# Kernel tuning notes

Measured on AMD Instinct MI355X. Metric: run time of the kernel, lower is better.

Reference implementation:

```python
import jax, jax.numpy as jnp
import numpy as np
from jax import lax

B, N, T, D_IN, D_OUT, LINK_LEN, EMBED = 32, 500, 12, 1, 64, 3, 10
C_WIN = 1            # x_window feature dim ((dim_in-1)%16==0 branch)
CNN_CH = D_OUT // 16  # 4 channels per topology CNN


def setup_inputs() -> dict:
    key = jax.random.key(0)
    ks = jax.random.split(key, 16)
    s = 0.1
    inp = {}
    inp["x"] = jax.random.normal(ks[0], (B, N, D_IN), jnp.float32)
    inp["x_window"] = jax.random.normal(ks[1], (B, T, N, C_WIN), jnp.float32)
    inp["node_embeddings"] = jax.random.normal(ks[2], (N, EMBED), jnp.float32)
    inp["adj"] = jax.random.uniform(ks[3], (N, N), jnp.float32)
    inp["MPG"] = jax.random.normal(ks[4], (B, T, N, N), jnp.float32)
    inp["bootstrap_idx"] = jnp.sort(jax.random.randint(ks[5], (3,), 0, T))
    inp["fixed_adj"] = 0
    inp["stay_cost"] = 1
    inp["jump_cost"] = 2
    inp["weights_pool"] = jax.random.normal(ks[6], (EMBED, LINK_LEN, D_IN, 3 * D_OUT // 4), jnp.float32) * s
    inp["window_weights_supra"] = jax.random.normal(ks[7], (EMBED, C_WIN, D_OUT // 8), jnp.float32) * s
    inp["window_weights_temporal"] = jax.random.normal(ks[8], (EMBED, C_WIN, D_OUT // 8), jnp.float32) * s
    inp["bias_pool"] = jax.random.normal(ks[9], (EMBED, D_OUT), jnp.float32) * s
    inp["T_param"] = jax.random.normal(ks[10], (T,), jnp.float32) * s
    inp["conv_mean_w"] = jax.random.normal(ks[11], (CNN_CH, T, 3, 3), jnp.float32) * s
    inp["conv_mean_b"] = jnp.zeros((CNN_CH,), jnp.float32)
    inp["conv_max_w"] = jax.random.normal(ks[12], (CNN_CH, T, 3, 3), jnp.float32) * s
    inp["conv_max_b"] = jnp.zeros((CNN_CH,), jnp.float32)
    return inp


def _conv2d(x, w, b):
    y = lax.conv_general_dilated(x, w, (1, 1), 'SAME',
                                 dimension_numbers=('NCHW', 'OIHW', 'NCHW'))
    return y + b[None, :, None, None]


def reference(x, x_window, node_embeddings, adj, MPG, bootstrap_idx, fixed_adj,
              stay_cost, jump_cost, weights_pool, window_weights_supra,
              window_weights_temporal, bias_pool, T_param,
              conv_mean_w, conv_mean_b, conv_max_w, conv_max_b):
    n = node_embeddings.shape[0]
    eye = jnp.eye(n, dtype=x.dtype)
    # adaptive adjacency from node embeddings, diagonal set to stay_cost
    s0 = jax.nn.relu(node_embeddings @ node_embeddings.T)
    s0 = jnp.where(eye > 0, jnp.asarray(stay_cost, x.dtype), s0)
    if fixed_adj == 1:
        S = adj * jnp.exp(s0)
    else:
        S = jax.nn.softmax(s0, axis=1)
    # faithful to torch broadcast: S[i,j] / sum_k S[j,k]
    S = S / jnp.sum(S, axis=1)
    # multi-hop supports: I, S, S@S, ...
    supports = [eye, S]
    for k in range(2, LINK_LEN):
        supports.append(S @ supports[-1])
    supports = jnp.stack(supports, axis=0)  # [K, N, N]
    # supra-laplacian: diagonal blocks S, strictly-upper blocks jump_cost*I
    F_b = bootstrap_idx.shape[0]  # 3 bootstrap layers
    supra = (jnp.kron(jnp.eye(F_b, dtype=x.dtype), S)
             + jnp.kron(jnp.triu(jnp.ones((F_b, F_b), x.dtype), 1),
                        jnp.asarray(jump_cost, x.dtype) * eye))
    # node-adaptive weights/bias
    weights = jnp.einsum('nd,dkio->nkio', node_embeddings, weights_pool)
    bias = node_embeddings @ bias_pool  # [N, D_OUT]
    # spatial graph conv
    x_s = jnp.einsum('knm,bmc->bnkc', supports, x)
    x_sconv = jnp.einsum('bnki,nkio->bno', x_s, weights)  # [B,N,48]
    # supra-laplacian window conv over bootstrap slices
    ww_s = jnp.einsum('nd,dio->nio', node_embeddings, window_weights_supra)
    xw = x_window[:, bootstrap_idx]            # [B, 3, N, c]
    b_sz = xw.shape[0]
    xw_flat = xw.reshape(b_sz, F_b * n, -1)    # [B, 3N, c]
    xws = jnp.einsum('bmi,mn->bni', xw_flat, supra).reshape(b_sz, F_b, n, -1)
    x_wconv_s = jnp.einsum('bfni,nio->bfno', xws, ww_s).mean(axis=1)  # [B,N,8]
    # temporal window conv
    ww_t = jnp.einsum('nd,dio->nio', node_embeddings, window_weights_temporal)
    x_wconv_t = jnp.einsum('btni,nio,t->bno', x_window, ww_t, T_param)  # [B,N,8]
    # topology CNNs (conv + relu + global mean / max pool)
    topo_mean = jax.nn.relu(_conv2d(MPG, conv_mean_w, conv_mean_b)).mean(axis=(2, 3))
    topo_max = jax.nn.relu(_conv2d(MPG, conv_max_w, conv_max_b)).max(axis=(2, 3))
    topo = jnp.concatenate([topo_mean, topo_max], axis=1)  # [B, 8]
    x_twconv_s = x_wconv_s * topo[:, None, :]
    return jnp.concatenate([x_sconv, x_twconv_s, x_wconv_t], axis=-1) + bias[None]
```

## Files before the change

### kernel.cpp

```cpp
#include <hip/hip_runtime.h>

#define NN 500
#define BB 32
#define TT 12
#define EMB 10

typedef short bf16x8 __attribute__((ext_vector_type(8)));
typedef float f32x16 __attribute__((ext_vector_type(16)));

__device__ __forceinline__ unsigned short f2bf(float x) {
    unsigned int u = __float_as_uint(x);
    u = (u + 0x7fffu + ((u >> 16) & 1u)) >> 16;
    return (unsigned short)u;
}

__global__ __launch_bounds__(256) void k_softmaxS(const float* __restrict__ E,
                                                  const int* __restrict__ stay,
                                                  float* __restrict__ S) {
    const int i = blockIdx.x;
    const int tid = threadIdx.x;
    __shared__ float row[NN];
    __shared__ float red[256];
    float ei[EMB];
#pragma unroll
    for (int d = 0; d < EMB; ++d) ei[d] = E[i * EMB + d];
    const float stayf = (float)stay[0];

    float lmax = -1e30f;
    for (int j = tid; j < NN; j += 256) {
        float acc = 0.f;
#pragma unroll
        for (int d = 0; d < EMB; ++d) acc += ei[d] * E[j * EMB + d];
        float v = acc > 0.f ? acc : 0.f;
        if (j == i) v = stayf;
        row[j] = v;
        lmax = fmaxf(lmax, v);
    }
    red[tid] = lmax;
    __syncthreads();
    for (int s = 128; s > 0; s >>= 1) {
        if (tid < s) red[tid] = fmaxf(red[tid], red[tid + s]);
        __syncthreads();
    }
    const float rmax = red[0];
    __syncthreads();

    float lsum = 0.f;
    for (int j = tid; j < NN; j += 256) {
        float e = __expf(row[j] - rmax);
        row[j] = e;
        lsum += e;
    }
    red[tid] = lsum;
    __syncthreads();
    for (int s = 128; s > 0; s >>= 1) {
        if (tid < s) red[tid] += red[tid + s];
        __syncthreads();
    }
    const float inv = 1.0f / red[0];
    for (int j = tid; j < NN; j += 256) S[i * NN + j] = row[j] * inv;
}

__global__ __launch_bounds__(256) void k_matvecS(const float* __restrict__ S,
                                                 const float* __restrict__ xin,
                                                 float* __restrict__ yout) {
    const int b = blockIdx.y;
    const int w = threadIdx.x >> 6;
    const int lane = threadIdx.x & 63;
    const int n = blockIdx.x * 4 + w;
    const float* xb = xin + b * NN;
    const float* Sr = S + n * NN;
    float acc = 0.f;
    for (int m = lane; m < NN; m += 64) acc += Sr[m] * xb[m];
#pragma unroll
    for (int off = 32; off > 0; off >>= 1) acc += __shfl_down(acc, off, 64);
    if (lane == 0) yout[b * NN + n] = acc;
}

__global__ __launch_bounds__(256) void k_smallpre(const float* __restrict__ E,
                                                  const float* __restrict__ wp,
                                                  const float* __restrict__ bp,
                                                  const float* __restrict__ wwsp,
                                                  const float* __restrict__ wwtp,
                                                  float* __restrict__ W,
                                                  float* __restrict__ biasN,
                                                  float* __restrict__ wws,
                                                  float* __restrict__ wwt) {
    const int n = blockIdx.x;
    const int tid = threadIdx.x;
    __shared__ float e[EMB];
    if (tid < EMB) e[tid] = E[n * EMB + tid];
    __syncthreads();
    if (tid < 144) {
        float acc = 0.f;
#pragma unroll
        for (int d = 0; d < EMB; ++d) acc += e[d] * wp[d * 144 + tid];
        W[n * 144 + tid] = acc;
    } else if (tid < 208) {
        const int o = tid - 144;
        float acc = 0.f;
#pragma unroll
        for (int d = 0; d < EMB; ++d) acc += e[d] * bp[d * 64 + o];
        biasN[n * 64 + o] = acc;
    } else if (tid < 216) {
        const int o = tid - 208;
        float acc = 0.f;
#pragma unroll
        for (int d = 0; d < EMB; ++d) acc += e[d] * wwsp[d * 8 + o];
        wws[n * 8 + o] = acc;
    } else if (tid < 224) {
        const int o = tid - 216;
        float acc = 0.f;
#pragma unroll
        for (int d = 0; d < EMB; ++d) acc += e[d] * wwtp[d * 8 + o];
        wwt[n * 8 + o] = acc;
    }
}

__global__ __launch_bounds__(128) void k_Mwsum(const float* __restrict__ xwin,
                                               const float* __restrict__ S,
                                               const int* __restrict__ bidx,
                                               const int* __restrict__ jumpc,
                                               const float* __restrict__ Tp,
                                               float* __restrict__ M,
                                               float* __restrict__ wsum) {
    const int b = blockIdx.y;
    const int n0 = blockIdx.x * 125;
    const int tid = threadIdx.x;
    __shared__ float xsf[NN];
    __shared__ float Tl[TT];
    const int t0 = bidx[0], t1 = bidx[1], t2 = bidx[2];
    if (tid < TT) Tl[tid] = Tp[tid];
    const float* xb = xwin + (size_t)b * TT * NN;
    for (int m = tid; m < NN; m += 128)
        xsf[m] = xb[t0 * NN + m] + xb[t1 * NN + m] + xb[t2 * NN + m];
    __syncthreads();
    if (tid < 125) {
        const int n = n0 + tid;
        float ws_ = 0.f;
#pragma unroll
        for (int t = 0; t < TT; ++t) ws_ += xb[t * NN + n] * Tl[t];
        const float jc = (float)jumpc[0];
        const float jterm = jc * (2.f * xb[t0 * NN + n] + xb[t1 * NN + n]);
        float acc = 0.f;
        for (int m = 0; m < NN; ++m) acc += xsf[m] * S[m * NN + n];
        M[b * NN + n] = (acc + jterm) * (1.f / 3.f);
        wsum[b * NN + n] = ws_;
    }
}

__global__ __launch_bounds__(256) void k_wpackB(const float* __restrict__ wm,
                                                const float* __restrict__ wx,
                                                unsigned short* __restrict__ wq) {
    const int i = blockIdx.x * 256 + threadIdx.x;
    if (i >= 9 * 64 * 8) return;
    const int j = i & 7;
    const int rest = i >> 3;
    const int lane = rest & 63;
    const int s = rest >> 6;
    const int kh = s / 3, kw = s - kh * 3;
    const int n = lane & 31;
    const int t = (lane >> 5) * 8 + j;
    float v = 0.f;
    if (t < TT) {
        if (n < 4) v = wm[((n * TT + t) * 3 + kh) * 3 + kw];
        else if (n < 8) v = wx[(((n - 4) * TT + t) * 3 + kh) * 3 + kw];
    }
    wq[i] = f2bf(v);
}

#define SLOTW 132
#define SLOTS (SLOTW * 24)
#define SLOTW32 (SLOTW * 12)

__global__ __launch_bounds__(256, 2) void k_conv(const float* __restrict__ MPG,
                                                 const unsigned short* __restrict__ wq,
                                                 const float* __restrict__ bmv,
                                                 const float* __restrict__ bxv,
                                                 float* __restrict__ partials) {
    const int b = blockIdx.y;
    const int cb = blockIdx.x >> 3;
    const int rb = blockIdx.x & 7;
    const int C0 = cb * 128;
    const int R0 = rb * 63;
    const int R1 = (R0 + 62 < NN - 1) ? R0 + 62 : NN - 1;
    const int tid = threadIdx.x;
    const int w = __builtin_amdgcn_readfirstlane(tid >> 6);
    const int lane = tid & 63;
    const int hi = lane >> 5;

    __shared__ unsigned short lsd[4 * SLOTS];
    __shared__ float wred[4][8][2];

    const float* basef = MPG + (size_t)b * TT * NN * NN;
    unsigned int* L32 = reinterpret_cast<unsigned int*>(lsd);

    bf16x8 bfq[9];
#pragma unroll
    for (int s = 0; s < 9; ++s)
        bfq[s] = *reinterpret_cast<const bf16x8*>(wq + (s * 64 + lane) * 8);

    bool uval[4], uco[4];
    size_t g0[4];
    int ud[4];
#pragma unroll
    for (int k = 0; k < 4; ++k) {
        const int f = tid + k * 256;
        uval[k] = (f < 6 * SLOTW);
        const int tp = uval[k] ? (f / SLOTW) : 0;
        const int sc = uval[k] ? (f - tp * SLOTW) : 0;
        const int gcol = C0 - 1 + sc;
        uco[k] = uval[k] && (gcol >= 0) && (gcol < NN);
        g0[k] = (size_t)(2 * tp) * (NN * NN) + (uco[k] ? gcol : 0);
        ud[k] = sc * 12 + tp;
    }

    for (int z = tid; z < 4 * SLOTW; z += 256) {
        const int s = z / SLOTW;
        const int sc = z - s * SLOTW;
        L32[s * SLOTW32 + sc * 12 + 6] = 0u;
        L32[s * SLOTW32 + sc * 12 + 7] = 0u;
    }

    const int ch = lane & 31;
    const float biasv = (ch < 4) ? bmv[ch] : ((ch < 8) ? bxv[ch - 4] : 0.f);
    const bool interior = (C0 + w * 32 + 31) < NN;
    float mkv[16];
#pragma unroll
    for (int i = 0; i < 16; ++i) {
        const int p = C0 + w * 32 + (i & 3) + 8 * (i >> 2) + 4 * hi;
        mkv[i] = (p < NN) ? 1.f : 0.f;
    }
    const int aoff = (w * 32 + ch) * 48 + hi * 16;

    auto STAGE_LOAD = [&](int rr, float (&v0)[4], float (&v1)[4]) {
        const bool rowok = (rr >= 0) && (rr < NN);
#pragma unroll
        for (int k = 0; k < 4; ++k) {
            v0[k] = 0.f; v1[k] = 0.f;
            if (uco[k] && rowok) {
                const size_t o = g0[k] + (size_t)rr * NN;
                v0[k] = basef[o];
                v1[k] = basef[o + (size_t)NN * NN];
            }
        }
    };
    auto STAGE_WRITE = [&](int rr, const float (&v0)[4], const float (&v1)[4]) {
        unsigned int* dst = L32 + ((rr + 1) & 3) * SLOTW32;
#pragma unroll
        for (int k = 0; k < 4; ++k) {
            if (uval[k]) {
                unsigned int r;
                asm("v_cvt_pk_bf16_f32 %0, %1, %2" : "=v"(r) : "v"(v0[k]), "v"(v1[k]));
                dst[ud[k]] = r;
            }
        }
    };

#pragma unroll
    for (int q = 0; q < 3; ++q) {
        float v0[4], v1[4];
        STAGE_LOAD(R0 - 1 + q, v0, v1);
        STAGE_WRITE(R0 - 1 + q, v0, v1);
    }
    __syncthreads();

    float sumv = 0.f, maxv = 0.f;

#pragma unroll 1
    for (int r = R0; r <= R1; ++r) {
        const int rr = r + 2;
        const bool do_stage = (rr <= R1 + 1);
        float v0[4], v1[4];
        if (do_stage) STAGE_LOAD(rr, v0, v1);

        f32x16 acc;
#pragma unroll
        for (int i = 0; i < 16; ++i) acc[i] = biasv;
#pragma unroll
        for (int kh = 0; kh < 3; ++kh) {
            const char* sb = reinterpret_cast<const char*>(lsd) + ((r + kh) & 3) * (SLOTS * 2);
#pragma unroll
            for (int kw = 0; kw < 3; ++kw) {
                const bf16x8 a = *reinterpret_cast<const bf16x8*>(sb + aoff + kw * 48);
                acc = __builtin_amdgcn_mfma_f32_32x32x16_bf16(a, bfq[kh * 3 + kw], acc, 0, 0, 0);
            }
        }

        if (interior) {
            float rs = 0.f;
#pragma unroll
            for (int i = 0; i < 16; ++i) rs += fmaxf(acc[i], 0.f);
            sumv += rs;
            float mm = acc[0];
#pragma unroll
            for (int i = 1; i < 16; ++i) mm = fmaxf(mm, acc[i]);
            maxv = fmaxf(maxv, mm);
        } else {
#pragma unroll
            for (int i = 0; i < 16; ++i) {
                const float v = fmaxf(acc[i], 0.f) * mkv[i];
                sumv += v;
                maxv = fmaxf(maxv, v);
            }
        }

        if (do_stage) STAGE_WRITE(rr, v0, v1);
        __syncthreads();
    }

    sumv += __shfl_xor(sumv, 32, 64);
    maxv = fmaxf(maxv, __shfl_xor(maxv, 32, 64));
    if (lane < 8) {
        wred[w][lane][0] = sumv;
        wred[w][lane][1] = maxv;
    }
    __syncthreads();
    if (tid < 8) {
        const float s = wred[0][tid][0] + wred[1][tid][0] + wred[2][tid][0] + wred[3][tid][0];
        const float mx = fmaxf(fmaxf(wred[0][tid][1], wred[1][tid][1]),
                               fmaxf(wred[2][tid][1], wred[3][tid][1]));
        partials[((size_t)b * 32 + blockIdx.x) * 8 + tid] = (tid < 4) ? s : mx;
    }
}

__global__ __launch_bounds__(256) void k_topo(const float* __restrict__ partials,
                                              float* __restrict__ topo) {
    const int b = blockIdx.x;
    const int tid = threadIdx.x;
    const int c = tid & 7;
    const int g = tid >> 3;
    float vs = 0.f, vm = 0.f;
    if (g < 32) {
        const float v = partials[((size_t)b * 32 + g) * 8 + c];
        vs = v;
        vm = v;
    }
    __shared__ float red[256];
    red[tid] = (c < 4) ? vs : vm;
    __syncthreads();
    for (int s = 16; s > 0; s >>= 1) {
        if (g < s) {
            const float a = red[tid];
            const float bv = red[tid + s * 8];
            red[tid] = (c < 4) ? (a + bv) : fmaxf(a, bv);
        }
        __syncthreads();
    }
    if (tid < 8) topo[b * 8 + tid] = (tid < 4) ? red[tid] * (1.f / (NN * (float)NN)) : red[tid];
}

__global__ __launch_bounds__(64) void k_out(const float* __restrict__ x,
                                            const float* __restrict__ y1,
                                            const float* __restrict__ y2,
                                            const float* __restrict__ W,
                                            const float* __restrict__ biasN,
                                            const float* __restrict__ wws,
                                            const float* __restrict__ wwt,
                                            const float* __restrict__ M,
                                            const float* __restrict__ wsum,
                                            const float* __restrict__ topo,
                                            float* __restrict__ out) {
    const int bn = blockIdx.x;
    const int b = bn / NN;
    const int n = bn - b * NN;
    const int o = threadIdx.x;
    float val;
    if (o < 48) {
        val = x[bn] * W[n * 144 + o] + y1[bn] * W[n * 144 + 48 + o] + y2[bn] * W[n * 144 + 96 + o];
    } else if (o < 56) {
        const int oo = o - 48;
        val = M[bn] * wws[n * 8 + oo] * topo[b * 8 + oo];
    } else {
        const int oo = o - 56;
        val = wsum[bn] * wwt[n * 8 + oo];
    }
    out[(size_t)bn * 64 + o] = val + biasN[n * 64 + o];
}

extern "C" void kernel_launch(void* const* d_in, const int* in_sizes, int n_in,
                              void* d_out, int out_size, void* d_ws, size_t ws_size,
                              hipStream_t stream) {
    const float* x    = (const float*)d_in[0];
    const float* xw   = (const float*)d_in[1];
    const float* E    = (const float*)d_in[2];
    const float* MPG  = (const float*)d_in[4];
    const int*   bidx = (const int*)d_in[5];
    const int*   stay = (const int*)d_in[7];
    const int*   jump = (const int*)d_in[8];
    const float* wp   = (const float*)d_in[9];
    const float* wwsp = (const float*)d_in[10];
    const float* wwtp = (const float*)d_in[11];
    const float* bp   = (const float*)d_in[12];
    const float* Tp   = (const float*)d_in[13];
    const float* cmw  = (const float*)d_in[14];
    const float* cmb  = (const float*)d_in[15];
    const float* cxw  = (const float*)d_in[16];
    const float* cxb  = (const float*)d_in[17];
    float* out = (float*)d_out;

    float* w = (float*)d_ws;
    float* S     = w;
    float* y1    = S + 250000;
    float* y2    = y1 + 16000;
    float* W     = y2 + 16000;
    float* biasN = W + 72000;
    float* wws   = biasN + 32000;
    float* wwt   = wws + 4000;
    float* M     = wwt + 4000;
    float* wsum  = M + 16000;
    float* parts = wsum + 16000;
    float* topo  = parts + 8192;
    float* wpckf = topo + 256;
    unsigned short* wq = (unsigned short*)wpckf;

    k_wpackB<<<18, 256, 0, stream>>>(cmw, cxw, wq);
    k_softmaxS<<<NN, 256, 0, stream>>>(E, stay, S);
    k_matvecS<<<dim3(125, BB), 256, 0, stream>>>(S, x, y1);
    k_matvecS<<<dim3(125, BB), 256, 0, stream>>>(S, y1, y2);
    k_smallpre<<<NN, 256, 0, stream>>>(E, wp, bp, wwsp, wwtp, W, biasN, wws, wwt);
    k_Mwsum<<<dim3(4, BB), 128, 0, stream>>>(xw, S, bidx, jump, Tp, M, wsum);
    k_conv<<<dim3(32, BB), 256, 0, stream>>>(MPG, wq, cmb, cxb, parts);
    k_topo<<<BB, 256, 0, stream>>>(parts, topo);
    k_out<<<BB * NN, 64, 0, stream>>>(x, y1, y2, W, biasN, wws, wwt, M, wsum, topo, out);
}
```

Baseline: 140.4 us.

## Process three output rows per iteration with an 8-slot LDS ring

The conv loop now computes three output rows per iteration. It loads five input rows of LDS fragments once and reuses them across the three rows' 27 MFMAs, and it stages three new rows per iteration. This cuts LDS reads and per-row barriers by about a factor of three. The last row block is shifted to start at NN-63 so every block runs exactly 21 iterations, and rows already covered by the previous block are masked out. In exchange, LDS use doubles to 8 slots, register pressure rises from holding 15 fragments plus 12 staged loads, and occupancy at two blocks per CU may be affected.

```diff
diff --git a/kernel.cpp b/kernel.cpp
--- a/kernel.cpp
+++ b/kernel.cpp
@@ -171,6 +171,7 @@
 
 #define SLOTW 132
 #define SLOTS (SLOTW * 24)
+#define SLOTB (SLOTS * 2)
 #define SLOTW32 (SLOTW * 12)
 
 __global__ __launch_bounds__(256, 2) void k_conv(const float* __restrict__ MPG,
@@ -182,14 +183,14 @@
     const int cb = blockIdx.x >> 3;
     const int rb = blockIdx.x & 7;
     const int C0 = cb * 128;
-    const int R0 = rb * 63;
-    const int R1 = (R0 + 62 < NN - 1) ? R0 + 62 : NN - 1;
+    const int rmin = rb * 63;
+    const int R0 = (rb < 7) ? rb * 63 : (NN - 63);
     const int tid = threadIdx.x;
     const int w = __builtin_amdgcn_readfirstlane(tid >> 6);
     const int lane = tid & 63;
     const int hi = lane >> 5;
 
-    __shared__ unsigned short lsd[4 * SLOTS];
+    __shared__ unsigned short lsd[8 * SLOTS];
     __shared__ float wred[4][8][2];
 
     const float* basef = MPG + (size_t)b * TT * NN * NN;
@@ -215,7 +216,7 @@
         ud[k] = sc * 12 + tp;
     }
 
-    for (int z = tid; z < 4 * SLOTW; z += 256) {
+    for (int z = tid; z < 8 * SLOTW; z += 256) {
         const int s = z / SLOTW;
         const int sc = z - s * SLOTW;
         L32[s * SLOTW32 + sc * 12 + 6] = 0u;
@@ -246,7 +247,7 @@
         }
     };
     auto STAGE_WRITE = [&](int rr, const float (&v0)[4], const float (&v1)[4]) {
-        unsigned int* dst = L32 + ((rr + 1) & 3) * SLOTW32;
+        unsigned int* dst = L32 + ((rr + 1) & 7) * SLOTW32;
 #pragma unroll
         for (int k = 0; k < 4; ++k) {
             if (uval[k]) {
@@ -258,7 +259,7 @@
     };
 
 #pragma unroll
-    for (int q = 0; q < 3; ++q) {
+    for (int q = 0; q < 5; ++q) {
         float v0[4], v1[4];
         STAGE_LOAD(R0 - 1 + q, v0, v1);
         STAGE_WRITE(R0 - 1 + q, v0, v1);
@@ -268,44 +269,64 @@
     float sumv = 0.f, maxv = 0.f;
 
 #pragma unroll 1
-    for (int r = R0; r <= R1; ++r) {
-        const int rr = r + 2;
-        const bool do_stage = (rr <= R1 + 1);
-        float v0[4], v1[4];
-        if (do_stage) STAGE_LOAD(rr, v0, v1);
-
-        f32x16 acc;
-#pragma unroll
-        for (int i = 0; i < 16; ++i) acc[i] = biasv;
-#pragma unroll
-        for (int kh = 0; kh < 3; ++kh) {
-            const char* sb = reinterpret_cast<const char*>(lsd) + ((r + kh) & 3) * (SLOTS * 2);
-#pragma unroll
-            for (int kw = 0; kw < 3; ++kw) {
-                const bf16x8 a = *reinterpret_cast<const bf16x8*>(sb + aoff + kw * 48);
-                acc = __builtin_amdgcn_mfma_f32_32x32x16_bf16(a, bfq[kh * 3 + kw], acc, 0, 0, 0);
+    for (int k21 = 0; k21 < 21; ++k21) {
+        const int r = R0 + 3 * k21;
+        const bool do_stage = (k21 < 20);
+
+        float v0[3][4], v1[3][4];
+        if (do_stage) {
+#pragma unroll
+            for (int q = 0; q < 3; ++q) STAGE_LOAD(r + 4 + q, v0[q], v1[q]);
+        }
+
+        bf16x8 F[5][3];
+#pragma unroll
+        for (int j = 0; j < 5; ++j) {
+            const char* sb = reinterpret_cast<const char*>(lsd) + ((r + j) & 7) * SLOTB;
+#pragma unroll
+            for (int kw = 0; kw < 3; ++kw)
+                F[j][kw] = *reinterpret_cast<const bf16x8*>(sb + aoff + kw * 48);
+        }
+
+#pragma unroll
+        for (int o = 0; o < 3; ++o) {
+            f32x16 acc;
+#pragma unroll
+            for (int i = 0; i < 16; ++i) acc[i] = biasv;
+#pragma unroll
+            for (int kh = 0; kh < 3; ++kh) {
+#pragma unroll
+                for (int kw = 0; kw < 3; ++kw)
+                    acc = __builtin_amdgcn_mfma_f32_32x32x16_bf16(F[o + kh][kw], bfq[kh * 3 + kw], acc, 0, 0, 0);
             }
-        }
-
-        if (interior) {
-            float rs = 0.f;
-#pragma unroll
-            for (int i = 0; i < 16; ++i) rs += fmaxf(acc[i], 0.f);
-            sumv += rs;
-            float mm = acc[0];
-#pragma unroll
-            for (int i = 1; i < 16; ++i) mm = fmaxf(mm, acc[i]);
-            maxv = fmaxf(maxv, mm);
-        } else {
-#pragma unroll
-            for (int i = 0; i < 16; ++i) {
-                const float v = fmaxf(acc[i], 0.f) * mkv[i];
-                sumv += v;
-                maxv = fmaxf(maxv, v);
+            const int ro = r + o;
+            if (interior && (ro >= rmin)) {
+                float rs = 0.f;
+#pragma unroll
+                for (int i = 0; i < 16; ++i) rs += fmaxf(acc[i], 0.f);
+                sumv += rs;
+                float mm = acc[0];
+#pragma unroll
+                for (int i = 1; i < 16; ++i) mm = fmaxf(mm, acc[i]);
+                maxv = fmaxf(maxv, mm);
+            } else {
+                const float rm = (ro >= rmin) ? 1.f : 0.f;
+                float rs = 0.f, rx = 0.f;
+#pragma unroll
+                for (int i = 0; i < 16; ++i) {
+                    const float v = fmaxf(acc[i], 0.f) * mkv[i];
+                    rs += v;
+                    rx = fmaxf(rx, v);
+                }
+                sumv += rm * rs;
+                maxv = fmaxf(maxv, rm * rx);
             }
         }
 
-        if (do_stage) STAGE_WRITE(rr, v0, v1);
+        if (do_stage) {
+#pragma unroll
+            for (int q = 0; q < 3; ++q) STAGE_WRITE(r + 4 + q, v0[q], v1[q]);
+        }
         __syncthreads();
     }
 
```

Result: slower. 153.7 us (+9.4%).

## Merge small preprocessing kernels into combined launches and split conv reduction accumulators

Applied to the files above, without the earlier changes.

Combines softmax adjacency, per-node weight generation and conv weight packing into one kernel selected by block index. It also folds the first matvec and the M/wsum computation into a single launch, cutting the launch count from nine to six. Separately, the conv epilogue now keeps 16 independent sum and max accumulators per lane instead of serial chains, shortening dependency chains at the cost of extra registers. The extra registers may reduce occupancy in k_conv, which is declared with launch bounds of 2 blocks.

```diff
diff --git a/kernel.cpp b/kernel.cpp
--- a/kernel.cpp
+++ b/kernel.cpp
@@ -14,51 +14,158 @@
     return (unsigned short)u;
 }
 
-__global__ __launch_bounds__(256) void k_softmaxS(const float* __restrict__ E,
-                                                  const int* __restrict__ stay,
-                                                  float* __restrict__ S) {
-    const int i = blockIdx.x;
+__global__ __launch_bounds__(256) void k_pre(const float* __restrict__ E,
+                                             const int* __restrict__ stay,
+                                             const float* __restrict__ wp,
+                                             const float* __restrict__ bp,
+                                             const float* __restrict__ wwsp,
+                                             const float* __restrict__ wwtp,
+                                             const float* __restrict__ wm,
+                                             const float* __restrict__ wx,
+                                             float* __restrict__ S,
+                                             float* __restrict__ W,
+                                             float* __restrict__ biasN,
+                                             float* __restrict__ wws,
+                                             float* __restrict__ wwt,
+                                             unsigned short* __restrict__ wq) {
+    const int bid = blockIdx.x;
     const int tid = threadIdx.x;
-    __shared__ float row[NN];
-    __shared__ float red[256];
-    float ei[EMB];
-#pragma unroll
-    for (int d = 0; d < EMB; ++d) ei[d] = E[i * EMB + d];
-    const float stayf = (float)stay[0];
-
-    float lmax = -1e30f;
-    for (int j = tid; j < NN; j += 256) {
+    if (bid < NN) {
+        __shared__ float row[NN];
+        __shared__ float red[256];
+        const int i = bid;
+        float ei[EMB];
+#pragma unroll
+        for (int d = 0; d < EMB; ++d) ei[d] = E[i * EMB + d];
+        const float stayf = (float)stay[0];
+
+        float lmax = -1e30f;
+        for (int j = tid; j < NN; j += 256) {
+            float acc = 0.f;
+#pragma unroll
+            for (int d = 0; d < EMB; ++d) acc += ei[d] * E[j * EMB + d];
+            float v = acc > 0.f ? acc : 0.f;
+            if (j == i) v = stayf;
+            row[j] = v;
+            lmax = fmaxf(lmax, v);
+        }
+        red[tid] = lmax;
+        __syncthreads();
+        for (int s = 128; s > 0; s >>= 1) {
+            if (tid < s) red[tid] = fmaxf(red[tid], red[tid + s]);
+            __syncthreads();
+        }
+        const float rmax = red[0];
+        __syncthreads();
+
+        float lsum = 0.f;
+        for (int j = tid; j < NN; j += 256) {
+            float e = __expf(row[j] - rmax);
+            row[j] = e;
+            lsum += e;
+        }
+        red[tid] = lsum;
+        __syncthreads();
+        for (int s = 128; s > 0; s >>= 1) {
+            if (tid < s) red[tid] += red[tid + s];
+            __syncthreads();
+        }
+        const float inv = 1.0f / red[0];
+        for (int j = tid; j < NN; j += 256) S[i * NN + j] = row[j] * inv;
+    } else if (bid < 2 * NN) {
+        const int n = bid - NN;
+        __shared__ float e[EMB];
+        if (tid < EMB) e[tid] = E[n * EMB + tid];
+        __syncthreads();
+        if (tid < 144) {
+            float acc = 0.f;
+#pragma unroll
+            for (int d = 0; d < EMB; ++d) acc += e[d] * wp[d * 144 + tid];
+            W[n * 144 + tid] = acc;
+        } else if (tid < 208) {
+            const int o = tid - 144;
+            float acc = 0.f;
+#pragma unroll
+            for (int d = 0; d < EMB; ++d) acc += e[d] * bp[d * 64 + o];
+            biasN[n * 64 + o] = acc;
+        } else if (tid < 216) {
+            const int o = tid - 208;
+            float acc = 0.f;
+#pragma unroll
+            for (int d = 0; d < EMB; ++d) acc += e[d] * wwsp[d * 8 + o];
+            wws[n * 8 + o] = acc;
+        } else if (tid < 224) {
+            const int o = tid - 216;
+            float acc = 0.f;
+#pragma unroll
+            for (int d = 0; d < EMB; ++d) acc += e[d] * wwtp[d * 8 + o];
+            wwt[n * 8 + o] = acc;
+        }
+    } else {
+        const int i = (bid - 2 * NN) * 256 + tid;
+        if (i < 9 * 64 * 8) {
+            const int j = i & 7;
+            const int rest = i >> 3;
+            const int lane = rest & 63;
+            const int s = rest >> 6;
+            const int kh = s / 3, kw = s - kh * 3;
+            const int n = lane & 31;
+            const int t = (lane >> 5) * 8 + j;
+            float v = 0.f;
+            if (t < TT) {
+                if (n < 4) v = wm[((n * TT + t) * 3 + kh) * 3 + kw];
+                else if (n < 8) v = wx[(((n - 4) * TT + t) * 3 + kh) * 3 + kw];
+            }
+            wq[i] = f2bf(v);
+        }
+    }
+}
+
+__global__ __launch_bounds__(256) void k_mv1(const float* __restrict__ S,
+                                             const float* __restrict__ x,
+                                             const float* __restrict__ xwin,
+                                             const int* __restrict__ bidx,
+                                             const int* __restrict__ jumpc,
+                                             const float* __restrict__ Tp,
+                                             float* __restrict__ y1,
+                                             float* __restrict__ M,
+                                             float* __restrict__ wsum) {
+    const int b = blockIdx.y;
+    const int tid = threadIdx.x;
+    if (blockIdx.x < 125) {
+        const int w = tid >> 6;
+        const int lane = tid & 63;
+        const int n = blockIdx.x * 4 + w;
+        const float* xb = x + b * NN;
+        const float* Sr = S + n * NN;
         float acc = 0.f;
-#pragma unroll
-        for (int d = 0; d < EMB; ++d) acc += ei[d] * E[j * EMB + d];
-        float v = acc > 0.f ? acc : 0.f;
-        if (j == i) v = stayf;
-        row[j] = v;
-        lmax = fmaxf(lmax, v);
-    }
-    red[tid] = lmax;
-    __syncthreads();
-    for (int s = 128; s > 0; s >>= 1) {
-        if (tid < s) red[tid] = fmaxf(red[tid], red[tid + s]);
-        __syncthreads();
-    }
-    const float rmax = red[0];
-    __syncthreads();
-
-    float lsum = 0.f;
-    for (int j = tid; j < NN; j += 256) {
-        float e = __expf(row[j] - rmax);
-        row[j] = e;
-        lsum += e;
-    }
-    red[tid] = lsum;
-    __syncthreads();
-    for (int s = 128; s > 0; s >>= 1) {
-        if (tid < s) red[tid] += red[tid + s];
-        __syncthreads();
-    }
-    const float inv = 1.0f / red[0];
-    for (int j = tid; j < NN; j += 256) S[i * NN + j] = row[j] * inv;
+        for (int m = lane; m < NN; m += 64) acc += Sr[m] * xb[m];
+#pragma unroll
+        for (int off = 32; off > 0; off >>= 1) acc += __shfl_down(acc, off, 64);
+        if (lane == 0) y1[b * NN + n] = acc;
+    } else {
+        const int n0 = (blockIdx.x - 125) * 125;
+        __shared__ float xsf[NN];
+        __shared__ float Tl[TT];
+        const int t0 = bidx[0], t1 = bidx[1], t2 = bidx[2];
+        if (tid < TT) Tl[tid] = Tp[tid];
+        const float* xb = xwin + (size_t)b * TT * NN;
+        for (int m = tid; m < NN; m += 256)
+            xsf[m] = xb[t0 * NN + m] + xb[t1 * NN + m] + xb[t2 * NN + m];
+        __syncthreads();
+        if (tid < 125) {
+            const int n = n0 + tid;
+            float ws_ = 0.f;
+#pragma unroll
+            for (int t = 0; t < TT; ++t) ws_ += xb[t * NN + n] * Tl[t];
+            const float jc = (float)jumpc[0];
+            const float jterm = jc * (2.f * xb[t0 * NN + n] + xb[t1 * NN + n]);
+            float acc = 0.f;
+            for (int m = 0; m < NN; ++m) acc += xsf[m] * S[m * NN + n];
+            M[b * NN + n] = (acc + jterm) * (1.f / 3.f);
+            wsum[b * NN + n] = ws_;
+        }
+    }
 }
 
 __global__ __launch_bounds__(256) void k_matvecS(const float* __restrict__ S,
@@ -75,98 +182,6 @@
 #pragma unroll
     for (int off = 32; off > 0; off >>= 1) acc += __shfl_down(acc, off, 64);
     if (lane == 0) yout[b * NN + n] = acc;
-}
-
-__global__ __launch_bounds__(256) void k_smallpre(const float* __restrict__ E,
-                                                  const float* __restrict__ wp,
-                                                  const float* __restrict__ bp,
-                                                  const float* __restrict__ wwsp,
-                                                  const float* __restrict__ wwtp,
-                                                  float* __restrict__ W,
-                                                  float* __restrict__ biasN,
-                                                  float* __restrict__ wws,
-                                                  float* __restrict__ wwt) {
-    const int n = blockIdx.x;
-    const int tid = threadIdx.x;
-    __shared__ float e[EMB];
-    if (tid < EMB) e[tid] = E[n * EMB + tid];
-    __syncthreads();
-    if (tid < 144) {
-        float acc = 0.f;
-#pragma unroll
-        for (int d = 0; d < EMB; ++d) acc += e[d] * wp[d * 144 + tid];
-        W[n * 144 + tid] = acc;
-    } else if (tid < 208) {
-        const int o = tid - 144;
-        float acc = 0.f;
-#pragma unroll
-        for (int d = 0; d < EMB; ++d) acc += e[d] * bp[d * 64 + o];
-        biasN[n * 64 + o] = acc;
-    } else if (tid < 216) {
-        const int o = tid - 208;
-        float acc = 0.f;
-#pragma unroll
-        for (int d = 0; d < EMB; ++d) acc += e[d] * wwsp[d * 8 + o];
-        wws[n * 8 + o] = acc;
-    } else if (tid < 224) {
-        const int o = tid - 216;
-        float acc = 0.f;
-#pragma unroll
-        for (int d = 0; d < EMB; ++d) acc += e[d] * wwtp[d * 8 + o];
-        wwt[n * 8 + o] = acc;
-    }
-}
-
-__global__ __launch_bounds__(128) void k_Mwsum(const float* __restrict__ xwin,
-                                               const float* __restrict__ S,
-                                               const int* __restrict__ bidx,
-                                               const int* __restrict__ jumpc,
-                                               const float* __restrict__ Tp,
-                                               float* __restrict__ M,
-                                               float* __restrict__ wsum) {
-    const int b = blockIdx.y;
-    const int n0 = blockIdx.x * 125;
-    const int tid = threadIdx.x;
-    __shared__ float xsf[NN];
-    __shared__ float Tl[TT];
-    const int t0 = bidx[0], t1 = bidx[1], t2 = bidx[2];
-    if (tid < TT) Tl[tid] = Tp[tid];
-    const float* xb = xwin + (size_t)b * TT * NN;
-    for (int m = tid; m < NN; m += 128)
-        xsf[m] = xb[t0 * NN + m] + xb[t1 * NN + m] + xb[t2 * NN + m];
-    __syncthreads();
-    if (tid < 125) {
-        const int n = n0 + tid;
-        float ws_ = 0.f;
-#pragma unroll
-        for (int t = 0; t < TT; ++t) ws_ += xb[t * NN + n] * Tl[t];
-        const float jc = (float)jumpc[0];
-        const float jterm = jc * (2.f * xb[t0 * NN + n] + xb[t1 * NN + n]);
-        float acc = 0.f;
-        for (int m = 0; m < NN; ++m) acc += xsf[m] * S[m * NN + n];
-        M[b * NN + n] = (acc + jterm) * (1.f / 3.f);
-        wsum[b * NN + n] = ws_;
-    }
-}
-
-__global__ __launch_bounds__(256) void k_wpackB(const float* __restrict__ wm,
-                                                const float* __restrict__ wx,
-                                                unsigned short* __restrict__ wq) {
-    const int i = blockIdx.x * 256 + threadIdx.x;
-    if (i >= 9 * 64 * 8) return;
-    const int j = i & 7;
-    const int rest = i >> 3;
-    const int lane = rest & 63;
-    const int s = rest >> 6;
-    const int kh = s / 3, kw = s - kh * 3;
-    const int n = lane & 31;
-    const int t = (lane >> 5) * 8 + j;
-    float v = 0.f;
-    if (t < TT) {
-        if (n < 4) v = wm[((n * TT + t) * 3 + kh) * 3 + kw];
-        else if (n < 8) v = wx[(((n - 4) * TT + t) * 3 + kh) * 3 + kw];
-    }
-    wq[i] = f2bf(v);
 }
 
 #define SLOTW 132
@@ -265,7 +280,9 @@
     }
     __syncthreads();
 
-    float sumv = 0.f, maxv = 0.f;
+    float s16[16], m16[16];
+#pragma unroll
+    for (int i = 0; i < 16; ++i) { s16[i] = 0.f; m16[i] = 0.f; }
 
 #pragma unroll 1
     for (int r = R0; r <= R1; ++r) {
@@ -288,25 +305,30 @@
         }
 
         if (interior) {
-            float rs = 0.f;
-#pragma unroll
-            for (int i = 0; i < 16; ++i) rs += fmaxf(acc[i], 0.f);
-            sumv += rs;
-            float mm = acc[0];
-#pragma unroll
-            for (int i = 1; i < 16; ++i) mm = fmaxf(mm, acc[i]);
-            maxv = fmaxf(maxv, mm);
+#pragma unroll
+            for (int i = 0; i < 16; ++i) {
+                const float v = fmaxf(acc[i], 0.f);
+                s16[i] += v;
+                m16[i] = fmaxf(m16[i], v);
+            }
         } else {
 #pragma unroll
             for (int i = 0; i < 16; ++i) {
                 const float v = fmaxf(acc[i], 0.f) * mkv[i];
-                sumv += v;
-                maxv = fmaxf(maxv, v);
+                s16[i] += v;
+                m16[i] = fmaxf(m16[i], v);
             }
         }
 
         if (do_stage) STAGE_WRITE(rr, v0, v1);
         __syncthreads();
+    }
+
+    float sumv = 0.f, maxv = 0.f;
+#pragma unroll
+    for (int i = 0; i < 16; ++i) {
+        sumv += s16[i];
+        maxv = fmaxf(maxv, m16[i]);
     }
 
     sumv += __shfl_xor(sumv, 32, 64);
@@ -414,12 +436,10 @@
     float* wpckf = topo + 256;
     unsigned short* wq = (unsigned short*)wpckf;
 
-    k_wpackB<<<18, 256, 0, stream>>>(cmw, cxw, wq);
-    k_softmaxS<<<NN, 256, 0, stream>>>(E, stay, S);
-    k_matvecS<<<dim3(125, BB), 256, 0, stream>>>(S, x, y1);
+    k_pre<<<2 * NN + 18, 256, 0, stream>>>(E, stay, wp, bp, wwsp, wwtp, cmw, cxw,
+                                           S, W, biasN, wws, wwt, wq);
+    k_mv1<<<dim3(129, BB), 256, 0, stream>>>(S, x, xw, bidx, jump, Tp, y1, M, wsum);
     k_matvecS<<<dim3(125, BB), 256, 0, stream>>>(S, y1, y2);
-    k_smallpre<<<NN, 256, 0, stream>>>(E, wp, bp, wwsp, wwtp, W, biasN, wws, wwt);
-    k_Mwsum<<<dim3(4, BB), 128, 0, stream>>>(xw, S, bidx, jump, Tp, M, wsum);
     k_conv<<<dim3(32, BB), 256, 0, stream>>>(MPG, wq, cmb, cxb, parts);
     k_topo<<<BB, 256, 0, stream>>>(parts, topo);
     k_out<<<BB * NN, 64, 0, stream>>>(x, y1, y2, W, biasN, wws, wwt, M, wsum, topo, out);
```

Measured after the change: 170.3 us. 21.3% more time.
